# Kernel tuning notes

Measured on AMD Instinct MI355X. Metric: run time of the kernel, lower is better.

Reference implementation:

```python
import jax, jax.numpy as jnp
import numpy as np
import math

N_LAYER = 4
D = 1024
H = 16
V = 32000
MAX_LEN = 2048
B = 2
L = 2048
EPS = 1e-6


def positional_encoding(max_len, dim):
    pos = jnp.arange(max_len, dtype=jnp.float32)[:, None]
    div = jnp.exp(jnp.arange(0, dim, 2, dtype=jnp.float32) * (-math.log(10000.0) / dim))
    ang = pos * div  # [max_len, dim//2]
    pe = jnp.zeros((max_len, dim), dtype=jnp.float32)
    pe = pe.at[:, 0::2].set(jnp.sin(ang)).at[:, 1::2].set(jnp.cos(ang))
    return pe


def setup_inputs() -> dict:
    key = jax.random.key(0)
    ks = jax.random.split(key, 20)
    s = 0.02
    inp = {
        "input_ids": jax.random.randint(ks[0], (B, L), 0, V),
        "embed": jax.random.normal(ks[1], (V, D), jnp.float32) * s,
        "Wq": jax.random.normal(ks[2], (N_LAYER, D, D), jnp.float32) * s,
        "bq": jnp.zeros((N_LAYER, D), jnp.float32),
        "Wk": jax.random.normal(ks[3], (N_LAYER, D, D), jnp.float32) * s,
        "bk": jnp.zeros((N_LAYER, D), jnp.float32),
        "Wv": jax.random.normal(ks[4], (N_LAYER, D, D), jnp.float32) * s,
        "bv": jnp.zeros((N_LAYER, D), jnp.float32),
        "Wo": jax.random.normal(ks[5], (N_LAYER, D, D), jnp.float32) * s,
        "bo": jnp.zeros((N_LAYER, D), jnp.float32),
        "Wproj": jax.random.normal(ks[6], (N_LAYER, D, 2 * D), jnp.float32) * s,
        "bproj": jnp.zeros((N_LAYER, 2 * D), jnp.float32),
        "Wup": jax.random.normal(ks[7], (N_LAYER, D, 2 * D), jnp.float32) * s,
        "bup": jnp.zeros((N_LAYER, 2 * D), jnp.float32),
        "Wdown": jax.random.normal(ks[8], (N_LAYER, 2 * D, D), jnp.float32) * s,
        "bdown": jnp.zeros((N_LAYER, D), jnp.float32),
        "gammas": jnp.ones((2 * N_LAYER, D), jnp.float32),
        "Wlogits": jax.random.normal(ks[9], (D, V), jnp.float32) * s,
        "blogits": jnp.zeros((V,), jnp.float32),
    }
    return inp


def rmsnorm(x, gamma):
    ms = jnp.mean(x * x, axis=-1, keepdims=True)
    return x * jax.lax.rsqrt(ms + EPS) * gamma


def attention(x, Wq, bq, Wk, bk, Wv, bv, Wo, bo):
    b, l, d = x.shape
    dh = d // H
    q = (x @ Wq + bq).reshape(b, l, H, dh)
    k = (x @ Wk + bk).reshape(b, l, H, dh)
    v = (x @ Wv + bv).reshape(b, l, H, dh)
    scores = jnp.einsum("blhd,bmhd->bhlm", q, k) / math.sqrt(dh)
    causal = jnp.tril(jnp.ones((l, l), dtype=bool))  # True where allowed
    scores = jnp.where(causal, scores, -jnp.inf)
    attn = jax.nn.softmax(scores, axis=-1)
    out = jnp.einsum("bhlm,bmhd->blhd", attn, v).reshape(b, l, d)
    return out @ Wo + bo


def ffn(x, Wproj, bproj, Wup, bup, Wdown, bdown):
    proj = x @ Wproj + bproj
    up = x @ Wup + bup
    gate = jax.nn.silu(proj * up)
    return gate @ Wdown + bdown


def reference(input_ids, embed, Wq, bq, Wk, bk, Wv, bv, Wo, bo,
              Wproj, bproj, Wup, bup, Wdown, bdown, gammas, Wlogits, blogits):
    b, l = input_ids.shape
    pe = positional_encoding(MAX_LEN, D)[:l]
    x = embed[input_ids] + pe
    for i in range(N_LAYER):
        x = x + attention(rmsnorm(x, gammas[2 * i]),
                          Wq[i], bq[i], Wk[i], bk[i], Wv[i], bv[i], Wo[i], bo[i])
        x = x + ffn(rmsnorm(x, gammas[2 * i + 1]),
                    Wproj[i], bproj[i], Wup[i], bup[i], Wdown[i], bdown[i])
    return x @ Wlogits + blogits
```

## Files before the change

kernel.cpp:

```cpp
#include <hip/hip_runtime.h>


typedef _Float16 f16;
typedef _Float16 v8h __attribute__((ext_vector_type(8)));
typedef float    v4f __attribute__((ext_vector_type(4)));

#define B_   2
#define L_   2048
#define D_   1024
#define H_   16
#define V_   32000
#define M_   (B_ * L_)

__device__ inline void g2l16(const void* g, void* l) {
  __builtin_amdgcn_global_load_lds((const __attribute__((address_space(1))) void*)g,
                                   (__attribute__((address_space(3))) void*)l,
                                   16, 0, 0);
}

template<int EPI>
__global__ __launch_bounds__(256) void gemm_bt(
    const f16* __restrict__ A, const f16* __restrict__ Bt,
    const float* __restrict__ bias, const float* resid, void* outp,
    int N, int K)
{
  __shared__ alignas(16) f16 As[128 * 32];
  __shared__ alignas(16) f16 Bs[128 * 32];

  const int tid  = threadIdx.x;
  const int wave = tid >> 6, lane = tid & 63;
  const int quad = lane >> 4, l16 = lane & 15;
  const long tm = (long)blockIdx.x * 128;
  const long tn = (long)blockIdx.y * 128;
  const int wm = (wave >> 1) * 64, wn = (wave & 1) * 64;

  v4f acc[4][4];
  for (int i = 0; i < 4; ++i)
    for (int j = 0; j < 4; ++j)
      for (int r = 0; r < 4; ++r) acc[i][j][r] = 0.f;

  for (int k0 = 0; k0 < K; k0 += 32) {
    __syncthreads();
    for (int h = 0; h < 2; ++h) {
      int c = h * 256 + wave * 64 + lane;
      long row = c >> 2;
      long koff = (long)k0 + (c & 3) * 8;
      g2l16(A  + (tm + row) * K + koff, As + (h * 256 + wave * 64) * 8);
      g2l16(Bt + (tn + row) * K + koff, Bs + (h * 256 + wave * 64) * 8);
    }
    __syncthreads();

    v8h a[4], b[4];
    for (int i = 0; i < 4; ++i) {
      a[i] = *(const v8h*)(As + (wm + i * 16 + l16) * 32 + quad * 8);
      b[i] = *(const v8h*)(Bs + (wn + i * 16 + l16) * 32 + quad * 8);
    }
    for (int i = 0; i < 4; ++i)
      for (int j = 0; j < 4; ++j)
        acc[i][j] = __builtin_amdgcn_mfma_f32_16x16x32_f16(a[i], b[j], acc[i][j], 0, 0, 0);
  }

  for (int i = 0; i < 4; ++i)
    for (int r = 0; r < 4; ++r) {
      long row = tm + wm + i * 16 + quad * 4 + r;
      for (int j = 0; j < 4; ++j) {
        long col = tn + wn + j * 16 + l16;
        float v = acc[i][j][r] + bias[col];
        long idx = row * (long)N + col;
        if (EPI == 0)      ((f16*)outp)[idx] = (f16)v;
        else if (EPI == 1) ((float*)outp)[idx] = resid[idx] + v;
        else               ((float*)outp)[idx] = v;
      }
    }
}

__global__ __launch_bounds__(256) void attn_k(const f16* __restrict__ qkv,
                                              f16* __restrict__ attno)
{
  const int qt = blockIdx.x;
  const int bh = blockIdx.y;
  const int b = bh >> 4, h = bh & 15;
  const int tid = threadIdx.x;
  const int wave = tid >> 6, lane = tid & 63;
  const int quad = lane >> 4, l16 = lane & 15;

  __shared__ alignas(16) f16 Ks[32 * 64];
  __shared__ alignas(16) f16 Vt[64 * 32];
  __shared__ alignas(16) f16 Ps[4][16 * 32];

  const f16* base = qkv + (size_t)b * L_ * 3072 + h * 64;

  const int qrow = qt * 64 + wave * 16 + l16;
  const v8h qf0 = *(const v8h*)(base + (size_t)qrow * 3072 + quad * 8);
  const v8h qf1 = *(const v8h*)(base + (size_t)qrow * 3072 + 32 + quad * 8);

  v4f of[4];
  float m_i[4], l_i[4];
  for (int n = 0; n < 4; ++n)
    for (int r = 0; r < 4; ++r) of[n][r] = 0.f;
  for (int r = 0; r < 4; ++r) { m_i[r] = -1e30f; l_i[r] = 0.f; }

  const int kr = tid >> 3, kc = tid & 7;
  const int nblocks = qt * 2 + 2;

  for (int kb = 0; kb < nblocks; ++kb) {
    const int key0 = kb * 32;
    __syncthreads();
    {
      const f16* ksrc = base + 1024 + (size_t)(key0 + kr) * 3072 + kc * 8;
      *(v8h*)(Ks + kr * 64 + kc * 8) = *(const v8h*)ksrc;
      const f16* vsrc = base + 2048 + (size_t)(key0 + kr) * 3072 + kc * 8;
      v8h vv = *(const v8h*)vsrc;
      for (int e = 0; e < 8; ++e) Vt[(kc * 8 + e) * 32 + kr] = vv[e];
    }
    __syncthreads();

    v4f sf[2];
    for (int s = 0; s < 2; ++s)
      for (int r = 0; r < 4; ++r) sf[s][r] = 0.f;
    for (int s = 0; s < 2; ++s) {
      v8h kf0 = *(const v8h*)(Ks + (s * 16 + l16) * 64 + quad * 8);
      v8h kf1 = *(const v8h*)(Ks + (s * 16 + l16) * 64 + 32 + quad * 8);
      sf[s] = __builtin_amdgcn_mfma_f32_16x16x32_f16(qf0, kf0, sf[s], 0, 0, 0);
      sf[s] = __builtin_amdgcn_mfma_f32_16x16x32_f16(qf1, kf1, sf[s], 0, 0, 0);
    }

    const int qg0 = qt * 64 + wave * 16 + quad * 4;
    float pv[2][4];
    for (int s = 0; s < 2; ++s)
      for (int r = 0; r < 4; ++r) {
        float sc = sf[s][r] * 0.125f;
        int kg = key0 + s * 16 + l16;
        if (kg > qg0 + r) sc = -1e30f;
        pv[s][r] = sc;
      }

    for (int r = 0; r < 4; ++r) {
      float mx = fmaxf(pv[0][r], pv[1][r]);
      for (int o = 8; o; o >>= 1) mx = fmaxf(mx, __shfl_xor(mx, o, 64));
      float mnew = fmaxf(m_i[r], mx);
      float alpha = expf(m_i[r] - mnew);
      m_i[r] = mnew;
      pv[0][r] = expf(pv[0][r] - mnew);
      pv[1][r] = expf(pv[1][r] - mnew);
      float rs = pv[0][r] + pv[1][r];
      for (int o = 8; o; o >>= 1) rs += __shfl_xor(rs, o, 64);
      l_i[r] = l_i[r] * alpha + rs;
      for (int n = 0; n < 4; ++n) of[n][r] *= alpha;
      Ps[wave][(quad * 4 + r) * 32 + l16]      = (f16)pv[0][r];
      Ps[wave][(quad * 4 + r) * 32 + 16 + l16] = (f16)pv[1][r];
    }
    __syncthreads();

    v8h pf = *(const v8h*)(&Ps[wave][0] + l16 * 32 + quad * 8);
    for (int n = 0; n < 4; ++n) {
      v8h vf = *(const v8h*)(Vt + (n * 16 + l16) * 32 + quad * 8);
      of[n] = __builtin_amdgcn_mfma_f32_16x16x32_f16(pf, vf, of[n], 0, 0, 0);
    }
  }

  const int q = qt * 64 + wave * 16 + quad * 4;
  f16* orow = attno + (size_t)b * L_ * 1024 + h * 64;
  for (int r = 0; r < 4; ++r) {
    float inv = 1.0f / l_i[r];
    for (int n = 0; n < 4; ++n)
      orow[(size_t)(q + r) * 1024 + n * 16 + l16] = (f16)(of[n][r] * inv);
  }
}

__global__ __launch_bounds__(256) void embed_pe(const int* __restrict__ ids,
                                                const float* __restrict__ emb,
                                                float* __restrict__ x)
{
  const int bl = blockIdx.x;
  const int l = bl & (L_ - 1);
  const int id = ids[bl];
  const float* e = emb + (size_t)id * D_;
  float* xr = x + (size_t)bl * D_;
  const int d0 = threadIdx.x * 4;
  for (int i = 0; i < 4; ++i) {
    int d = d0 + i;
    int p = d >> 1;
    float ang = (float)l * expf((float)(2 * p) * -0.008994473019508053f);
    float pe = (d & 1) ? cosf(ang) : sinf(ang);
    xr[d] = e[d] + pe;
  }
}

__global__ __launch_bounds__(256) void rmsnorm_k(const float* __restrict__ x,
                                                 const float* __restrict__ gamma,
                                                 f16* __restrict__ y)
{
  const int row = blockIdx.x;
  const float4 v = ((const float4*)(x + (size_t)row * D_))[threadIdx.x];
  float s = v.x * v.x + v.y * v.y + v.z * v.z + v.w * v.w;
  for (int o = 32; o; o >>= 1) s += __shfl_xor(s, o, 64);
  __shared__ float red[4];
  const int wave = threadIdx.x >> 6;
  if ((threadIdx.x & 63) == 0) red[wave] = s;
  __syncthreads();
  const float tot = red[0] + red[1] + red[2] + red[3];
  const float scale = rsqrtf(tot * (1.0f / D_) + 1e-6f);
  f16* yr = y + (size_t)row * D_;
  const int d = threadIdx.x * 4;
  yr[d]     = (f16)(v.x * scale * gamma[d]);
  yr[d + 1] = (f16)(v.y * scale * gamma[d + 1]);
  yr[d + 2] = (f16)(v.z * scale * gamma[d + 2]);
  yr[d + 3] = (f16)(v.w * scale * gamma[d + 3]);
}

__global__ __launch_bounds__(256) void transpose_cvt(const float* __restrict__ in,
                                                     f16* __restrict__ out,
                                                     int K, int N)
{
  __shared__ float tile[32][33];
  const int r = threadIdx.x >> 5, c = threadIdx.x & 31;
  const size_t bk = (size_t)blockIdx.y * 32;
  const size_t bn = (size_t)blockIdx.x * 32;
  for (int i = 0; i < 32; i += 8)
    tile[r + i][c] = in[(bk + r + i) * N + bn + c];
  __syncthreads();
  for (int i = 0; i < 32; i += 8)
    out[(bn + r + i) * K + bk + c] = (f16)tile[c][r + i];
}

__global__ __launch_bounds__(256) void gate_k(const f16* __restrict__ PU,
                                              f16* __restrict__ g)
{
  const int e = (blockIdx.x * 256 + threadIdx.x) * 4;
  const int row = e >> 11, col = e & 2047;
  const f16* p = PU + (size_t)row * 4096 + col;
  const f16* u = p + 2048;
  f16* go = g + (size_t)row * 2048 + col;
  for (int i = 0; i < 4; ++i) {
    float z = (float)p[i] * (float)u[i];
    go[i] = (f16)(z / (1.0f + expf(-z)));
  }
}

__global__ __launch_bounds__(256) void cast_k(const float* __restrict__ x,
                                              f16* __restrict__ y)
{
  const int i = blockIdx.x * 1024 + threadIdx.x * 4;
  const float4 v = *(const float4*)(x + i);
  y[i] = (f16)v.x; y[i + 1] = (f16)v.y; y[i + 2] = (f16)v.z; y[i + 3] = (f16)v.w;
}

__global__ __launch_bounds__(256) void build_biases(
    const float* bq, const float* bk, const float* bv,
    const float* bp, const float* bu, float* bqkv, float* bpu)
{
  const int i = blockIdx.x;
  for (int j = threadIdx.x; j < 3072; j += 256)
    bqkv[i * 3072 + j] = j < 1024 ? bq[i * 1024 + j]
                       : j < 2048 ? bk[i * 1024 + j - 1024]
                                  : bv[i * 1024 + j - 2048];
  for (int j = threadIdx.x; j < 4096; j += 256)
    bpu[i * 4096 + j] = j < 2048 ? bp[i * 2048 + j] : bu[i * 2048 + j - 2048];
}

extern "C" void kernel_launch(void* const* d_in, const int* in_sizes, int n_in,
                              void* d_out, int out_size, void* d_ws, size_t ws_size,
                              hipStream_t stream)
{
  (void)in_sizes; (void)n_in; (void)out_size; (void)ws_size;
  const int*   ids     = (const int*)  d_in[0];
  const float* embed   = (const float*)d_in[1];
  const float* Wq      = (const float*)d_in[2];
  const float* bq      = (const float*)d_in[3];
  const float* Wk      = (const float*)d_in[4];
  const float* bk      = (const float*)d_in[5];
  const float* Wv      = (const float*)d_in[6];
  const float* bv      = (const float*)d_in[7];
  const float* Wo      = (const float*)d_in[8];
  const float* bo      = (const float*)d_in[9];
  const float* Wproj   = (const float*)d_in[10];
  const float* bproj   = (const float*)d_in[11];
  const float* Wup     = (const float*)d_in[12];
  const float* bup     = (const float*)d_in[13];
  const float* Wdown   = (const float*)d_in[14];
  const float* bdown   = (const float*)d_in[15];
  const float* gammas  = (const float*)d_in[16];
  const float* Wlogits = (const float*)d_in[17];
  const float* blogits = (const float*)d_in[18];

  char* ws = (char*)d_ws;
  float* x    = (float*)ws;
  f16*   y    = (f16*)  (ws + 16777216);
  float* bqkv = (float*)(ws + 25165824);
  float* bpu  = (float*)(ws + 25214976);
  f16*   wbuf = (f16*)  (ws + 25280512);
  f16* wqkvT  = wbuf;
  f16* woT    = wbuf + 3145728;
  f16* wpuT   = wbuf + 4194304;
  f16* wdownT = wbuf + 8388608;

  char* ob  = (char*)d_out;
  f16* qkv   = (f16*)ob;
  f16* attno = (f16*)(ob + 25165824);
  f16* PU    = (f16*)(ob + 33554432);
  f16* g     = (f16*)(ob + 67108864);

  embed_pe<<<M_, 256, 0, stream>>>(ids, embed, x);
  build_biases<<<4, 256, 0, stream>>>(bq, bk, bv, bproj, bup, bqkv, bpu);

  for (int i = 0; i < 4; ++i) {
    const float* Wqi = Wq + (size_t)i * 1048576;
    const float* Wki = Wk + (size_t)i * 1048576;
    const float* Wvi = Wv + (size_t)i * 1048576;
    const float* Woi = Wo + (size_t)i * 1048576;
    const float* Wpi = Wproj + (size_t)i * 2097152;
    const float* Wui = Wup   + (size_t)i * 2097152;
    const float* Wdi = Wdown + (size_t)i * 2097152;

    transpose_cvt<<<dim3(32, 32), 256, 0, stream>>>(Wqi, wqkvT,                1024, 1024);
    transpose_cvt<<<dim3(32, 32), 256, 0, stream>>>(Wki, wqkvT + 1048576,      1024, 1024);
    transpose_cvt<<<dim3(32, 32), 256, 0, stream>>>(Wvi, wqkvT + 2097152,      1024, 1024);
    transpose_cvt<<<dim3(32, 32), 256, 0, stream>>>(Woi, woT,                  1024, 1024);
    transpose_cvt<<<dim3(64, 32), 256, 0, stream>>>(Wpi, wpuT,                 1024, 2048);
    transpose_cvt<<<dim3(64, 32), 256, 0, stream>>>(Wui, wpuT + 2097152,       1024, 2048);
    transpose_cvt<<<dim3(32, 64), 256, 0, stream>>>(Wdi, wdownT,               2048, 1024);

    rmsnorm_k<<<M_, 256, 0, stream>>>(x, gammas + (size_t)(2 * i) * 1024, y);
    gemm_bt<0><<<dim3(32, 24), 256, 0, stream>>>(y, wqkvT, bqkv + i * 3072, nullptr, qkv, 3072, 1024);
    attn_k<<<dim3(32, 32), 256, 0, stream>>>(qkv, attno);
    gemm_bt<1><<<dim3(32, 8), 256, 0, stream>>>(attno, woT, bo + i * 1024, x, x, 1024, 1024);

    rmsnorm_k<<<M_, 256, 0, stream>>>(x, gammas + (size_t)(2 * i + 1) * 1024, y);
    gemm_bt<0><<<dim3(32, 32), 256, 0, stream>>>(y, wpuT, bpu + i * 4096, nullptr, PU, 4096, 1024);
    gate_k<<<8192, 256, 0, stream>>>(PU, g);
    gemm_bt<1><<<dim3(32, 8), 256, 0, stream>>>(g, wdownT, bdown + i * 1024, x, x, 1024, 2048);
  }

  transpose_cvt<<<dim3(1000, 32), 256, 0, stream>>>(Wlogits, wbuf, 1024, 32000);
  cast_k<<<M_, 256, 0, stream>>>(x, y);
  gemm_bt<2><<<dim3(32, 250), 256, 0, stream>>>(y, wbuf, blogits, nullptr, (float*)d_out, 32000, 1024);
}
```

Baseline: 2.995 ms.

## Swizzle GEMM blocks across XCDs, add 128x64 GEMM, swizzle attention LDS

Adds XCD-aware workgroup remapping to the GEMMs so neighbouring tiles land on the same XCD and share L2. Adds a 128x64-tile GEMM for the N=1024 output projections, doubling the workgroup count from 256 to 512 to fill more CUs. In attention, query tiles are processed longest-first to balance the causal workload, and the K and V^T shared-memory layouts are XOR-swizzled to reduce bank conflicts. Smaller tiles give less data reuse per workgroup, and the swizzle adds index arithmetic.

```diff
diff --git a/kernel.cpp b/kernel.cpp
--- a/kernel.cpp
+++ b/kernel.cpp
@@ -18,6 +18,16 @@
                                    16, 0, 0);
 }
 
+__device__ inline void xcd_swz(int& bx, int& by, int gx, int gy) {
+  int nwg  = gx * gy;
+  int orig = by * gx + bx;
+  int q = nwg >> 3, r = nwg & 7;
+  int xcd = orig & 7, local = orig >> 3;
+  int swz = (xcd < r ? xcd * (q + 1) : r * (q + 1) + (xcd - r) * q) + local;
+  bx = swz % gx;
+  by = swz / gx;
+}
+
 template<int EPI>
 __global__ __launch_bounds__(256) void gemm_bt(
     const f16* __restrict__ A, const f16* __restrict__ Bt,
@@ -27,11 +37,14 @@
   __shared__ alignas(16) f16 As[128 * 32];
   __shared__ alignas(16) f16 Bs[128 * 32];
 
+  int bx = blockIdx.x, by = blockIdx.y;
+  xcd_swz(bx, by, (int)gridDim.x, (int)gridDim.y);
+
   const int tid  = threadIdx.x;
   const int wave = tid >> 6, lane = tid & 63;
   const int quad = lane >> 4, l16 = lane & 15;
-  const long tm = (long)blockIdx.x * 128;
-  const long tn = (long)blockIdx.y * 128;
+  const long tm = (long)bx * 128;
+  const long tn = (long)by * 128;
   const int wm = (wave >> 1) * 64, wn = (wave & 1) * 64;
 
   v4f acc[4][4];
@@ -74,10 +87,74 @@
     }
 }
 
+template<int EPI>
+__global__ __launch_bounds__(256) void gemm64_bt(
+    const f16* __restrict__ A, const f16* __restrict__ Bt,
+    const float* __restrict__ bias, const float* resid, void* outp,
+    int N, int K)
+{
+  __shared__ alignas(16) f16 As[128 * 32];
+  __shared__ alignas(16) f16 Bs[64 * 32];
+
+  int bx = blockIdx.x, by = blockIdx.y;
+  xcd_swz(bx, by, (int)gridDim.x, (int)gridDim.y);
+
+  const int tid  = threadIdx.x;
+  const int wave = tid >> 6, lane = tid & 63;
+  const int quad = lane >> 4, l16 = lane & 15;
+  const long tm = (long)bx * 128;
+  const long tn = (long)by * 64;
+  const int wm = (wave >> 1) * 64, wn = (wave & 1) * 32;
+
+  v4f acc[4][2];
+  for (int i = 0; i < 4; ++i)
+    for (int j = 0; j < 2; ++j)
+      for (int r = 0; r < 4; ++r) acc[i][j][r] = 0.f;
+
+  for (int k0 = 0; k0 < K; k0 += 32) {
+    __syncthreads();
+    for (int h = 0; h < 2; ++h) {
+      int c = h * 256 + wave * 64 + lane;
+      long row = c >> 2;
+      long koff = (long)k0 + (c & 3) * 8;
+      g2l16(A + (tm + row) * K + koff, As + (h * 256 + wave * 64) * 8);
+    }
+    {
+      int c = wave * 64 + lane;
+      long row = c >> 2;
+      long koff = (long)k0 + (c & 3) * 8;
+      g2l16(Bt + (tn + row) * K + koff, Bs + (wave * 64) * 8);
+    }
+    __syncthreads();
+
+    v8h a[4], b[2];
+    for (int i = 0; i < 4; ++i)
+      a[i] = *(const v8h*)(As + (wm + i * 16 + l16) * 32 + quad * 8);
+    for (int j = 0; j < 2; ++j)
+      b[j] = *(const v8h*)(Bs + (wn + j * 16 + l16) * 32 + quad * 8);
+    for (int i = 0; i < 4; ++i)
+      for (int j = 0; j < 2; ++j)
+        acc[i][j] = __builtin_amdgcn_mfma_f32_16x16x32_f16(a[i], b[j], acc[i][j], 0, 0, 0);
+  }
+
+  for (int i = 0; i < 4; ++i)
+    for (int r = 0; r < 4; ++r) {
+      long row = tm + wm + i * 16 + quad * 4 + r;
+      for (int j = 0; j < 2; ++j) {
+        long col = tn + wn + j * 16 + l16;
+        float v = acc[i][j][r] + bias[col];
+        long idx = row * (long)N + col;
+        if (EPI == 0)      ((f16*)outp)[idx] = (f16)v;
+        else if (EPI == 1) ((float*)outp)[idx] = resid[idx] + v;
+        else               ((float*)outp)[idx] = v;
+      }
+    }
+}
+
 __global__ __launch_bounds__(256) void attn_k(const f16* __restrict__ qkv,
                                               f16* __restrict__ attno)
 {
-  const int qt = blockIdx.x;
+  const int qt = (int)gridDim.x - 1 - blockIdx.x;
   const int bh = blockIdx.y;
   const int b = bh >> 4, h = bh & 15;
   const int tid = threadIdx.x;
@@ -101,6 +178,7 @@
   for (int r = 0; r < 4; ++r) { m_i[r] = -1e30f; l_i[r] = 0.f; }
 
   const int kr = tid >> 3, kc = tid & 7;
+  const int vkr = tid & 31, vkc = tid >> 5;
   const int nblocks = qt * 2 + 2;
 
   for (int kb = 0; kb < nblocks; ++kb) {
@@ -108,10 +186,14 @@
     __syncthreads();
     {
       const f16* ksrc = base + 1024 + (size_t)(key0 + kr) * 3072 + kc * 8;
-      *(v8h*)(Ks + kr * 64 + kc * 8) = *(const v8h*)ksrc;
-      const f16* vsrc = base + 2048 + (size_t)(key0 + kr) * 3072 + kc * 8;
+      *(v8h*)(Ks + kr * 64 + ((kc ^ (kr & 7)) * 8)) = *(const v8h*)ksrc;
+      const f16* vsrc = base + 2048 + (size_t)(key0 + vkr) * 3072 + vkc * 8;
       v8h vv = *(const v8h*)vsrc;
-      for (int e = 0; e < 8; ++e) Vt[(kc * 8 + e) * 32 + kr] = vv[e];
+      const int vc = vkr >> 3, vs = vkr & 7;
+      for (int e = 0; e < 8; ++e) {
+        int row = vkc * 8 + e;
+        Vt[row * 32 + ((vc ^ ((row >> 1) & 3)) * 8) + vs] = vv[e];
+      }
     }
     __syncthreads();
 
@@ -119,8 +201,9 @@
     for (int s = 0; s < 2; ++s)
       for (int r = 0; r < 4; ++r) sf[s][r] = 0.f;
     for (int s = 0; s < 2; ++s) {
-      v8h kf0 = *(const v8h*)(Ks + (s * 16 + l16) * 64 + quad * 8);
-      v8h kf1 = *(const v8h*)(Ks + (s * 16 + l16) * 64 + 32 + quad * 8);
+      int row = s * 16 + l16;
+      v8h kf0 = *(const v8h*)(Ks + row * 64 + ((quad ^ (row & 7)) * 8));
+      v8h kf1 = *(const v8h*)(Ks + row * 64 + (((4 + quad) ^ (row & 7)) * 8));
       sf[s] = __builtin_amdgcn_mfma_f32_16x16x32_f16(qf0, kf0, sf[s], 0, 0, 0);
       sf[s] = __builtin_amdgcn_mfma_f32_16x16x32_f16(qf1, kf1, sf[s], 0, 0, 0);
     }
@@ -154,7 +237,8 @@
 
     v8h pf = *(const v8h*)(&Ps[wave][0] + l16 * 32 + quad * 8);
     for (int n = 0; n < 4; ++n) {
-      v8h vf = *(const v8h*)(Vt + (n * 16 + l16) * 32 + quad * 8);
+      int vrow = n * 16 + l16;
+      v8h vf = *(const v8h*)(Vt + vrow * 32 + ((quad ^ ((vrow >> 1) & 3)) * 8));
       of[n] = __builtin_amdgcn_mfma_f32_16x16x32_f16(pf, vf, of[n], 0, 0, 0);
     }
   }
@@ -324,12 +408,12 @@
     rmsnorm_k<<<M_, 256, 0, stream>>>(x, gammas + (size_t)(2 * i) * 1024, y);
     gemm_bt<0><<<dim3(32, 24), 256, 0, stream>>>(y, wqkvT, bqkv + i * 3072, nullptr, qkv, 3072, 1024);
     attn_k<<<dim3(32, 32), 256, 0, stream>>>(qkv, attno);
-    gemm_bt<1><<<dim3(32, 8), 256, 0, stream>>>(attno, woT, bo + i * 1024, x, x, 1024, 1024);
+    gemm64_bt<1><<<dim3(32, 16), 256, 0, stream>>>(attno, woT, bo + i * 1024, x, x, 1024, 1024);
 
     rmsnorm_k<<<M_, 256, 0, stream>>>(x, gammas + (size_t)(2 * i + 1) * 1024, y);
     gemm_bt<0><<<dim3(32, 32), 256, 0, stream>>>(y, wpuT, bpu + i * 4096, nullptr, PU, 4096, 1024);
     gate_k<<<8192, 256, 0, stream>>>(PU, g);
-    gemm_bt<1><<<dim3(32, 8), 256, 0, stream>>>(g, wdownT, bdown + i * 1024, x, x, 1024, 2048);
+    gemm64_bt<1><<<dim3(32, 16), 256, 0, stream>>>(g, wdownT, bdown + i * 1024, x, x, 1024, 2048);
   }
 
   transpose_cvt<<<dim3(1000, 32), 256, 0, stream>>>(Wlogits, wbuf, 1024, 32000);
```

Measured after the change: 2.756 ms. 1.09x faster.
